# Performance work log

Measured on AMD Instinct MI355X. Metric: run time of the kernel, lower is better.

Reference implementation:

```python
import jax, jax.numpy as jnp
import numpy as np

N_QUBITS = 14
W_MUL = (2.0 ** 0.5) * (5.0 ** -0.5)  # he_std = gain * 5**-0.5, lrmul = 1
TWO_PI = 2.0 * np.pi


def _rx(t):
    c = jnp.cos(t / 2); s = jnp.sin(t / 2)
    return jnp.stack([jnp.stack([c + 0j, -1j * s]), jnp.stack([-1j * s, c + 0j])])


def _ry(t):
    c = jnp.cos(t / 2); s = jnp.sin(t / 2)
    return jnp.stack([jnp.stack([c + 0j, -s + 0j]), jnp.stack([s + 0j, c + 0j])])


def _rz(t):
    e = jnp.exp(-0.5j * t); z = jnp.zeros_like(e)
    return jnp.stack([jnp.stack([e, z]), jnp.stack([z, jnp.conj(e)])])


def _apply_1q(state, gate, q):
    # state: (B,) + (2,)*n ; apply 2x2 gate on qubit q (axis q+1)
    ax = q + 1
    out = jnp.tensordot(gate, state, axes=([1], [ax]))  # new qubit axis at front
    return jnp.moveaxis(out, 0, ax)


_CNOT = jnp.array([[1, 0, 0, 0],
                   [0, 1, 0, 0],
                   [0, 0, 0, 1],
                   [0, 0, 1, 0]], dtype=jnp.complex64).reshape(2, 2, 2, 2)


def _apply_cnot(state, c, t):
    # _CNOT indices: [out_c, out_t, in_c, in_t]
    out = jnp.tensordot(_CNOT, state, axes=([2, 3], [c + 1, t + 1]))
    return jnp.moveaxis(out, (0, 1), (c + 1, t + 1))


def _rot_layer(state, params, gates):
    # per-qubit triple of rotations: params[3*i + j] for gate j on qubit i
    for i in range(N_QUBITS):
        for j, g in enumerate(gates):
            state = _apply_1q(state, g(params[3 * i + j]), i)
    return state


def _ring_of_cnot(state):
    for i in range(N_QUBITS):
        state = _apply_cnot(state, i, (i + 1) % N_QUBITS)
    return state


def _forward(x_real, x_imag, weight):
    n = N_QUBITS
    B = x_real.shape[0]
    psi = (x_real + 1j * x_imag).astype(jnp.complex64).reshape((B,) + (2,) * n)
    w = weight * W_MUL
    layers = [(_rx, _ry, _rz),  # XYZLayer
              (_ry, _rz, _ry),  # YZYLayer
              (_rz, _ry, _rx),  # ZYXLayer
              (_rx, _rz, _rx),  # XZXLayer
              (_ry, _rz, _ry)]  # YZYLayer
    for li, gates in enumerate(layers):
        psi = _rot_layer(psi, w[3 * n * li: 3 * n * (li + 1)], gates)
        if li < len(layers) - 1:
            psi = _ring_of_cnot(psi)
    Z = jnp.array([[1, 0], [0, -1]], dtype=jnp.complex64)
    zpsi = _apply_1q(psi, Z, 0)
    # <psi| Z_0 |psi> (original: conj(psi) row-vector @ (Z_0 psi) column-vector, take real)
    ev = jnp.sum(jnp.conj(psi) * zpsi, axis=tuple(range(1, n + 1))).real
    return ev.reshape(B, 1)  # matches torch (B,1,1).squeeze(-1)


def setup_inputs() -> dict:
    key = jax.random.key(0)
    k1, k2, k3 = jax.random.split(key, 3)
    B = 512
    dim = 2 ** N_QUBITS
    x_real = jax.random.normal(k1, (B, 1, dim), dtype=jnp.float32)
    x_imag = jax.random.normal(k2, (B, 1, dim), dtype=jnp.float32)
    weight = jax.random.uniform(k3, (15 * N_QUBITS,), dtype=jnp.float32) * TWO_PI
    return {"x_real": x_real, "x_imag": x_imag, "weight": weight}


def reference(x_real, x_imag, weight):
    return _forward(x_real, x_imag, weight)
```

## Files before the change

### kernel.cpp

```cpp
#include <hip/hip_runtime.h>
#include <hip/hip_bf16.h>

#define NQ   14
#define DIM  16384
#define BLK  1024
#define WMUL 0.6324555320336759f

typedef float v2f __attribute__((ext_vector_type(2)));

struct C2 { float x, y; };
__device__ inline C2 cmulc(C2 a, C2 b){ return C2{a.x*b.x - a.y*b.y, a.x*b.y + a.y*b.x}; }
__device__ inline C2 caddc(C2 a, C2 b){ return C2{a.x+b.x, a.y+b.y}; }
__device__ inline void mm2(const C2* a, const C2* b, C2* o) {
    o[0] = caddc(cmulc(a[0],b[0]), cmulc(a[1],b[2]));
    o[1] = caddc(cmulc(a[0],b[1]), cmulc(a[1],b[3]));
    o[2] = caddc(cmulc(a[2],b[0]), cmulc(a[3],b[2]));
    o[3] = caddc(cmulc(a[2],b[1]), cmulc(a[3],b[3]));
}
__device__ inline void build_gate(int ty, float t, C2* g) {
    float sn, cs;
    __sincosf(0.5f * t, &sn, &cs);
    if (ty == 0) {
        g[0] = C2{cs, 0.f}; g[1] = C2{0.f, -sn};
        g[2] = C2{0.f, -sn}; g[3] = C2{cs, 0.f};
    } else if (ty == 1) {
        g[0] = C2{cs, 0.f}; g[1] = C2{-sn, 0.f};
        g[2] = C2{sn, 0.f}; g[3] = C2{cs, 0.f};
    } else {
        g[0] = C2{cs, -sn}; g[1] = C2{0.f, 0.f};
        g[2] = C2{0.f, 0.f}; g[3] = C2{cs, sn};
    }
}
__device__ const int TYPES[5][3] = {
    {0,1,2},
    {1,2,1},
    {2,1,0},
    {0,2,0},
    {1,2,1},
};

__device__ inline constexpr uint32_t slotf(uint32_t i){
    return i ^ (((i>>4) ^ (i>>8) ^ (i>>12)) & 15u);
}
template<int B> __device__ inline uint32_t ins0(uint32_t t){
    return ((t & ~((1u<<B)-1u)) << 1) | (t & ((1u<<B)-1u));
}
template<int B0,int B1,int B2> __device__ inline uint32_t expand3(uint32_t t){
    return ins0<B2>(ins0<B1>(ins0<B0>(t)));
}
template<int B0,int B1,int B2> __device__ inline constexpr uint32_t rmask3(int r){
    return ((r&1)?(1u<<B0):0u) | ((r&2)?(1u<<B1):0u) | ((r&4)?(1u<<B2):0u);
}

template<int J>
__device__ inline void rot8(v2f* v, const v2f* __restrict__ g){
    const v2f a00=g[0], b00=g[1], a01=g[2], b01=g[3];
    const v2f a10=g[4], b10=g[5], a11=g[6], b11=g[7];
    #pragma unroll
    for (int r = 0; r < 8; ++r){
        if (!(r & (1 << J))) {
            v2f x0 = v[r], x1 = v[r | (1 << J)];
            v2f s0 = x0.yx, s1 = x1.yx;
            v2f y0 = a00*x0 + b00*s0 + a01*x1 + b01*s1;
            v2f y1 = a10*x0 + b10*s0 + a11*x1 + b11*s1;
            v[r] = y0; v[r | (1<<J)] = y1;
        }
    }
}
template<int C, int T>
__device__ inline void cnot8(v2f* v){
    #pragma unroll
    for (int r = 0; r < 8; ++r){
        if ((r & (1 << C)) && !(r & (1 << T))) {
            v2f tt = v[r]; v[r] = v[r | (1 << T)]; v[r | (1 << T)] = tt;
        }
    }
}

__global__ __launch_bounds__(BLK) void qsim_kernel(
        const float* __restrict__ xr, const float* __restrict__ xi,
        const float* __restrict__ w, float* __restrict__ out) {
    __shared__ v2f s[DIM];
    __shared__ v2f gmp[5 * NQ * 8];
    __shared__ float red[BLK / 64];

    const int b   = blockIdx.x;
    const uint32_t tid = threadIdx.x;

    if (tid < 5 * NQ) {
        const int li = tid / NQ, q = tid % NQ;
        C2 M[4], G[4], T[4];
        #pragma unroll
        for (int j = 0; j < 3; ++j) {
            float t = w[3 * NQ * li + 3 * q + j] * WMUL;
            build_gate(TYPES[li][j], t, G);
            if (j == 0) { M[0]=G[0]; M[1]=G[1]; M[2]=G[2]; M[3]=G[3]; }
            else { mm2(G, M, T); M[0]=T[0]; M[1]=T[1]; M[2]=T[2]; M[3]=T[3]; }
        }
        #pragma unroll
        for (int k = 0; k < 4; ++k) {
            gmp[tid * 8 + k * 2 + 0] = v2f{ M[k].x, M[k].x};
            gmp[tid * 8 + k * 2 + 1] = v2f{-M[k].y, M[k].y};
        }
    }
    __syncthreads();

    const float* xrb = xr + (size_t)b * DIM;
    const float* xib = xi + (size_t)b * DIM;

    #define GMP(li, q) (&gmp[((li) * NQ + (q)) * 8])

    #define PASS(B0, B1, B2, ...)                                                  \
        _Pragma("unroll 1")                                                        \
        for (uint32_t sl = 0; sl < 2; ++sl) {                                      \
            const uint32_t t  = tid + sl * BLK;                                    \
            const uint32_t sb = slotf(expand3<B0,B1,B2>(t));                       \
            v2f v[8];                                                              \
            _Pragma("unroll")                                                      \
            for (int r = 0; r < 8; ++r)                                            \
                v[r] = s[sb ^ slotf(rmask3<B0,B1,B2>(r))];                         \
            __VA_ARGS__                                                            \
            _Pragma("unroll")                                                      \
            for (int r = 0; r < 8; ++r)                                            \
                s[sb ^ slotf(rmask3<B0,B1,B2>(r))] = v[r];                         \
        }                                                                          \
        __syncthreads();

    #pragma unroll 1
    for (int li = 0; li < 3; ++li) {
        #pragma unroll 1
        for (uint32_t sl = 0; sl < 2; ++sl) {
            const uint32_t t = tid + sl * BLK;
            v2f v[8];
            if (li == 0) {
                #pragma unroll
                for (int r = 0; r < 8; ++r) {
                    uint32_t i = t | ((uint32_t)r << 11);
                    v[r] = v2f{xrb[i], xib[i]};
                }
            } else {
                const uint32_t sb = slotf(expand3<11,12,13>(t));
                #pragma unroll
                for (int r = 0; r < 8; ++r)
                    v[r] = s[sb ^ slotf(rmask3<11,12,13>(r))];
            }
            rot8<2>(v, GMP(li,0)); rot8<1>(v, GMP(li,1)); rot8<0>(v, GMP(li,2));
            cnot8<2,1>(v); cnot8<1,0>(v);
            const uint32_t sb = slotf(expand3<11,12,13>(t));
            #pragma unroll
            for (int r = 0; r < 8; ++r)
                s[sb ^ slotf(rmask3<11,12,13>(r))] = v[r];
        }
        __syncthreads();

        PASS(9,10,11, rot8<1>(v, GMP(li,3));  rot8<0>(v, GMP(li,4));  cnot8<2,1>(v); cnot8<1,0>(v);)
        PASS(7,8,9,   rot8<1>(v, GMP(li,5));  rot8<0>(v, GMP(li,6));  cnot8<2,1>(v); cnot8<1,0>(v);)
        PASS(5,6,7,   rot8<1>(v, GMP(li,7));  rot8<0>(v, GMP(li,8));  cnot8<2,1>(v); cnot8<1,0>(v);)
        PASS(3,4,5,   rot8<1>(v, GMP(li,9));  rot8<0>(v, GMP(li,10)); cnot8<2,1>(v); cnot8<1,0>(v);)
        PASS(1,2,3,   rot8<1>(v, GMP(li,11)); rot8<0>(v, GMP(li,12)); cnot8<2,1>(v); cnot8<1,0>(v);)
        PASS(0,1,13,  rot8<0>(v, GMP(li,13)); cnot8<1,0>(v); cnot8<0,2>(v);)
    }

    PASS(11,12,13, rot8<2>(v, GMP(3,0));  rot8<1>(v, GMP(3,1));  rot8<0>(v, GMP(3,2));
                   cnot8<2,1>(v); cnot8<1,0>(v);
                   rot8<1>(v, GMP(4,1));)
    PASS(9,10,11,  rot8<1>(v, GMP(3,3));  rot8<0>(v, GMP(3,4));
                   cnot8<2,1>(v); cnot8<1,0>(v);
                   rot8<2>(v, GMP(4,2));  rot8<1>(v, GMP(4,3));)
    PASS(7,8,9,    rot8<1>(v, GMP(3,5));  rot8<0>(v, GMP(3,6));
                   cnot8<2,1>(v); cnot8<1,0>(v);
                   rot8<2>(v, GMP(4,4));  rot8<1>(v, GMP(4,5));)
    PASS(5,6,7,    rot8<1>(v, GMP(3,7));  rot8<0>(v, GMP(3,8));
                   cnot8<2,1>(v); cnot8<1,0>(v);
                   rot8<2>(v, GMP(4,6));  rot8<1>(v, GMP(4,7));)
    PASS(3,4,5,    rot8<1>(v, GMP(3,9));  rot8<0>(v, GMP(3,10));
                   cnot8<2,1>(v); cnot8<1,0>(v);
                   rot8<2>(v, GMP(4,8));  rot8<1>(v, GMP(4,9));)
    PASS(1,2,3,    rot8<1>(v, GMP(3,11)); rot8<0>(v, GMP(3,12));
                   cnot8<2,1>(v); cnot8<1,0>(v);
                   rot8<2>(v, GMP(4,10)); rot8<1>(v, GMP(4,11));)

    float local = 0.f;
    #pragma unroll 1
    for (uint32_t sl = 0; sl < 2; ++sl) {
        const uint32_t t  = tid + sl * BLK;
        const uint32_t sb = slotf(expand3<0,1,13>(t));
        v2f v[8];
        #pragma unroll
        for (int r = 0; r < 8; ++r)
            v[r] = s[sb ^ slotf(rmask3<0,1,13>(r))];
        rot8<0>(v, GMP(3,13));
        cnot8<1,0>(v); cnot8<0,2>(v);
        rot8<1>(v, GMP(4,12)); rot8<0>(v, GMP(4,13)); rot8<2>(v, GMP(4,0));
        #pragma unroll
        for (int r = 0; r < 8; ++r) {
            v2f p = v[r] * v[r];
            float m = p.x + p.y;
            local += (r & 4) ? -m : m;
        }
    }

    #pragma unroll
    for (int off = 32; off > 0; off >>= 1) local += __shfl_down(local, off);
    const int lane = tid & 63, wid = tid >> 6;
    if (lane == 0) red[wid] = local;
    __syncthreads();
    if (tid == 0) {
        float t = 0.f;
        #pragma unroll
        for (int k = 0; k < BLK / 64; ++k) t += red[k];
        out[b] = t;
    }
}

extern "C" void kernel_launch(void* const* d_in, const int* in_sizes, int n_in,
                              void* d_out, int out_size, void* d_ws, size_t ws_size,
                              hipStream_t stream) {
    const float* xr = (const float*)d_in[0];
    const float* xi = (const float*)d_in[1];
    const float* w  = (const float*)d_in[2];
    float* out = (float*)d_out;
    const int B = out_size;
    qsim_kernel<<<B, BLK, 0, stream>>>(xr, xi, w, out);
}
```

Before: 130.0 us.

## Fold final rotation layer into a qubit-0 measurement quadratic form

```diff
diff --git a/kernel.cpp b/kernel.cpp
--- a/kernel.cpp
+++ b/kernel.cpp
@@ -82,6 +82,7 @@
         const float* __restrict__ w, float* __restrict__ out) {
     __shared__ v2f s[DIM];
     __shared__ v2f gmp[5 * NQ * 8];
+    __shared__ float meas[4];
     __shared__ float red[BLK / 64];
 
     const int b   = blockIdx.x;
@@ -101,6 +102,12 @@
         for (int k = 0; k < 4; ++k) {
             gmp[tid * 8 + k * 2 + 0] = v2f{ M[k].x, M[k].x};
             gmp[tid * 8 + k * 2 + 1] = v2f{-M[k].y, M[k].y};
+        }
+        if (tid == 4 * NQ + 0) {
+            meas[0] = M[0].x*M[0].x + M[0].y*M[0].y - (M[2].x*M[2].x + M[2].y*M[2].y);
+            meas[1] = M[1].x*M[1].x + M[1].y*M[1].y - (M[3].x*M[3].x + M[3].y*M[3].y);
+            meas[2] = (M[0].x*M[1].x + M[0].y*M[1].y) - (M[2].x*M[3].x + M[2].y*M[3].y);
+            meas[3] = (M[0].x*M[1].y - M[0].y*M[1].x) - (M[2].x*M[3].y - M[2].y*M[3].x);
         }
     }
     __syncthreads();
@@ -126,8 +133,10 @@
         }                                                                          \
         __syncthreads();
 
+    float local = 0.f;
+
     #pragma unroll 1
-    for (int li = 0; li < 3; ++li) {
+    for (int li = 0; li < 4; ++li) {
         #pragma unroll 1
         for (uint32_t sl = 0; sl < 2; ++sl) {
             const uint32_t t = tid + sl * BLK;
@@ -158,46 +167,35 @@
         PASS(5,6,7,   rot8<1>(v, GMP(li,7));  rot8<0>(v, GMP(li,8));  cnot8<2,1>(v); cnot8<1,0>(v);)
         PASS(3,4,5,   rot8<1>(v, GMP(li,9));  rot8<0>(v, GMP(li,10)); cnot8<2,1>(v); cnot8<1,0>(v);)
         PASS(1,2,3,   rot8<1>(v, GMP(li,11)); rot8<0>(v, GMP(li,12)); cnot8<2,1>(v); cnot8<1,0>(v);)
-        PASS(0,1,13,  rot8<0>(v, GMP(li,13)); cnot8<1,0>(v); cnot8<0,2>(v);)
-    }
-
-    PASS(11,12,13, rot8<2>(v, GMP(3,0));  rot8<1>(v, GMP(3,1));  rot8<0>(v, GMP(3,2));
-                   cnot8<2,1>(v); cnot8<1,0>(v);
-                   rot8<1>(v, GMP(4,1));)
-    PASS(9,10,11,  rot8<1>(v, GMP(3,3));  rot8<0>(v, GMP(3,4));
-                   cnot8<2,1>(v); cnot8<1,0>(v);
-                   rot8<2>(v, GMP(4,2));  rot8<1>(v, GMP(4,3));)
-    PASS(7,8,9,    rot8<1>(v, GMP(3,5));  rot8<0>(v, GMP(3,6));
-                   cnot8<2,1>(v); cnot8<1,0>(v);
-                   rot8<2>(v, GMP(4,4));  rot8<1>(v, GMP(4,5));)
-    PASS(5,6,7,    rot8<1>(v, GMP(3,7));  rot8<0>(v, GMP(3,8));
-                   cnot8<2,1>(v); cnot8<1,0>(v);
-                   rot8<2>(v, GMP(4,6));  rot8<1>(v, GMP(4,7));)
-    PASS(3,4,5,    rot8<1>(v, GMP(3,9));  rot8<0>(v, GMP(3,10));
-                   cnot8<2,1>(v); cnot8<1,0>(v);
-                   rot8<2>(v, GMP(4,8));  rot8<1>(v, GMP(4,9));)
-    PASS(1,2,3,    rot8<1>(v, GMP(3,11)); rot8<0>(v, GMP(3,12));
-                   cnot8<2,1>(v); cnot8<1,0>(v);
-                   rot8<2>(v, GMP(4,10)); rot8<1>(v, GMP(4,11));)
-
-    float local = 0.f;
-    #pragma unroll 1
-    for (uint32_t sl = 0; sl < 2; ++sl) {
-        const uint32_t t  = tid + sl * BLK;
-        const uint32_t sb = slotf(expand3<0,1,13>(t));
-        v2f v[8];
-        #pragma unroll
-        for (int r = 0; r < 8; ++r)
-            v[r] = s[sb ^ slotf(rmask3<0,1,13>(r))];
-        rot8<0>(v, GMP(3,13));
-        cnot8<1,0>(v); cnot8<0,2>(v);
-        rot8<1>(v, GMP(4,12)); rot8<0>(v, GMP(4,13)); rot8<2>(v, GMP(4,0));
-        #pragma unroll
-        for (int r = 0; r < 8; ++r) {
-            v2f p = v[r] * v[r];
-            float m = p.x + p.y;
-            local += (r & 4) ? -m : m;
-        }
+
+        #pragma unroll 1
+        for (uint32_t sl = 0; sl < 2; ++sl) {
+            const uint32_t t  = tid + sl * BLK;
+            const uint32_t sb = slotf(expand3<0,1,13>(t));
+            v2f v[8];
+            #pragma unroll
+            for (int r = 0; r < 8; ++r)
+                v[r] = s[sb ^ slotf(rmask3<0,1,13>(r))];
+            rot8<0>(v, GMP(li,13));
+            cnot8<1,0>(v); cnot8<0,2>(v);
+            if (li < 3) {
+                #pragma unroll
+                for (int r = 0; r < 8; ++r)
+                    s[sb ^ slotf(rmask3<0,1,13>(r))] = v[r];
+            } else {
+                const float mA = meas[0], mB = meas[1], mP = meas[2], mQ = meas[3];
+                #pragma unroll
+                for (int r = 0; r < 4; ++r) {
+                    v2f a0 = v[r], a1 = v[r | 4];
+                    float n0 = a0.x*a0.x + a0.y*a0.y;
+                    float n1 = a1.x*a1.x + a1.y*a1.y;
+                    float u  = a0.x*a1.x + a0.y*a1.y;
+                    float vv = a0.x*a1.y - a0.y*a1.x;
+                    local += mA*n0 + mB*n1 + 2.f*(mP*u - mQ*vv);
+                }
+            }
+        }
+        if (li < 3) __syncthreads();
     }
 
     #pragma unroll
```

After: 115.2 us. 11.4% less time.
